# Kernel optimization log

Hardware: AMD Instinct MI355X
Metric: run time of the kernel (lower is better)

The kernel has to match this reference:

```python
import jax, jax.numpy as jnp
import numpy as np

N, D, H, B = 8192, 1024, 100, 32  # pairs, key dim, MLP hidden, batch_size


def setup_inputs() -> dict:
    key = jax.random.key(0)
    ks = jax.random.split(key, 6)
    q = jax.random.normal(ks[0], (N, D), jnp.float32)
    x = jax.random.normal(ks[1], (N, D), jnp.float32)
    b = jax.random.randint(ks[2], (N,), 0, B, dtype=jnp.int32)
    y = jax.random.randint(ks[3], (N,), 0, 2, dtype=jnp.int32)
    # Encoder params: Linear(2D -> H), ReLU, Linear(H -> 1)
    W1 = jax.random.normal(ks[4], (2 * D, H), jnp.float32) * (1.0 / np.sqrt(2 * D))
    b1 = jnp.zeros((H,), jnp.float32)
    W2 = jax.random.normal(ks[5], (H, 1), jnp.float32) * (1.0 / np.sqrt(H))
    b2 = jnp.zeros((1,), jnp.float32)
    return {"b": b, "q": q, "x": x, "y": y, "W1": W1, "b1": b1, "W2": W2, "b2": b2}


def reference(b, q, x, y, W1, b1, W2, b2):
    # Encoder: score per (query, key) pair
    inp = jnp.concatenate([q, x], axis=1)              # (N, 2D)
    h = jax.nn.relu(inp @ W1 + b1)                     # (N, H)
    s = (h @ W2 + b2)[:, 0]                            # (N,)

    n = s.shape[0]
    r = jnp.arange(n)
    yb = y.astype(bool)
    # pair mask: same batch element, differing labels, upper triangle
    m = (b[:, None] == b[None, :]) \
        & (yb[:, None] ^ yb[None, :]) \
        & (r[:, None] < r[None, :])                    # (N, N) bool

    d = s[:, None] - s[None, :]                        # (N, N) score diffs (logits)
    z = y.astype(jnp.float32)[:, None]                 # row label broadcast as target
    # stable BCE-with-logits, masked mean (== BCEWithLogitsLoss over selected pairs)
    bce = jnp.maximum(d, 0.0) - d * z + jnp.log1p(jnp.exp(-jnp.abs(d)))
    mf = m.astype(jnp.float32)
    loss = jnp.sum(bce * mf) / jnp.sum(mf)
    return loss
```

## Files before the change

kernel.cpp:

```cpp
#include <hip/hip_runtime.h>
#include <math.h>
#include <stdint.h>

#define NN 8192
#define DD 1024
#define KT 2048
#define HH 100
#define HP 128
#define LCAP 512
#define NB 32
#define BKC 64
#define NCH (KT / BKC)

typedef short bf16x8 __attribute__((ext_vector_type(8)));
typedef short bf16x4 __attribute__((ext_vector_type(4)));
typedef float f32x4 __attribute__((ext_vector_type(4)));

__device__ __forceinline__ short f2bf(float f) {
    uint32_t u = __builtin_bit_cast(uint32_t, f);
    u += 0x7FFF + ((u >> 16) & 1);
    return (short)(u >> 16);
}

__global__ __launch_bounds__(256) void prep_w1p(const float* __restrict__ W1,
                                                short* __restrict__ w1p)
{
    __shared__ float ld[32][104];
    const int t  = threadIdx.x;
    const int k0 = blockIdx.x * 32;
    for (int i = t; i < 32 * HH; i += 256) {
        const int kk = i / HH, cc = i - kk * HH;
        ld[kk][cc] = W1[(size_t)(k0 + kk) * HH + cc];
    }
    __syncthreads();
    for (int idx = t; idx < 512; idx += 256) {
        const int tt = idx >> 6, l = idx & 63;
        const int lr = l & 15, lg = l >> 4;
        const int col = tt * 16 + lr;
        bf16x8 r;
#pragma unroll
        for (int j = 0; j < 8; ++j)
            r[j] = (col < HH) ? f2bf(ld[lg * 8 + j][col]) : (short)0;
        *(bf16x8*)(w1p + ((size_t)(blockIdx.x * 8 + tt) * 64 + l) * 8) = r;
    }
}

__global__ __launch_bounds__(256) void encoder_mfma(
    const float* __restrict__ q, const float* __restrict__ x,
    const short* __restrict__ w1p,
    const float* __restrict__ b1, const float* __restrict__ W2,
    const float* __restrict__ b2,
    const int* __restrict__ bidx, const int* __restrict__ y,
    float* __restrict__ sp, float* __restrict__ sn,
    int* __restrict__ cnt1, int* __restrict__ cnt0)
{
    __shared__ short As[3][16][64];
    __shared__ float fold[4][16];
    const int t  = threadIdx.x;
    const int w  = t >> 6;
    const int l  = t & 63;
    const int lr = l & 15;
    const int lg = l >> 4;
    const int r0 = blockIdx.x * 16;

    const int srow  = t >> 4;
    const int sslot = t & 15;
    const int wslot = sslot ^ srow;
    const float* qb = q + (size_t)(r0 + srow) * DD + sslot * 4;
    const float* xb = x + (size_t)(r0 + srow) * DD + sslot * 4;
    auto aptr = [&](int c) -> const float* {
        const int kc = c * BKC;
        return (kc < DD) ? (qb + kc) : (xb + (kc - DD));
    };
    auto stage = [&](int buf, const float4& v) {
        bf16x4 s;
        s[0] = f2bf(v.x); s[1] = f2bf(v.y); s[2] = f2bf(v.z); s[3] = f2bf(v.w);
        *(bf16x4*)&As[buf][srow][wslot * 4] = s;
    };

    const int p0 = ((2 * lg)     ^ lr) * 4;
    const int p1 = ((2 * lg + 1) ^ lr) * 4;
    const int p2 = ((2 * lg + 8) ^ lr) * 4;
    const int p3 = ((2 * lg + 9) ^ lr) * 4;

    const short* pB = w1p + ((size_t)(2 * w) * 64 + l) * 8;
#define LOADB(c, x0, x1, x2, x3)                           \
    { const size_t e_ = (size_t)(c) * 8192;                \
      x0 = *(const bf16x8*)(pB + e_);                      \
      x1 = *(const bf16x8*)(pB + e_ + 4096);               \
      x2 = *(const bf16x8*)(pB + e_ + 512);                \
      x3 = *(const bf16x8*)(pB + e_ + 4096 + 512); }

    f32x4 acc0 = (f32x4)0.f, acc1 = (f32x4)0.f;
    bf16x8 bA0, bA1, bA2, bA3, bB0, bB1, bB2, bB3;

#define FRAGS_MFMA(rb, b0, b1_, b2_, b3_)                                   \
    { const short* ar = &As[rb][lr][0];                                     \
      bf16x4 g0 = *(const bf16x4*)(ar + p0);                                \
      bf16x4 g1 = *(const bf16x4*)(ar + p1);                                \
      bf16x4 g2 = *(const bf16x4*)(ar + p2);                                \
      bf16x4 g3 = *(const bf16x4*)(ar + p3);                                \
      bf16x8 aa0 = __builtin_shufflevector(g0, g1, 0,1,2,3,4,5,6,7);        \
      bf16x8 aa1 = __builtin_shufflevector(g2, g3, 0,1,2,3,4,5,6,7);        \
      acc0 = __builtin_amdgcn_mfma_f32_16x16x32_bf16(aa0, b0,  acc0, 0,0,0);\
      acc0 = __builtin_amdgcn_mfma_f32_16x16x32_bf16(aa1, b1_, acc0, 0,0,0);\
      acc1 = __builtin_amdgcn_mfma_f32_16x16x32_bf16(aa0, b2_, acc1, 0,0,0);\
      acc1 = __builtin_amdgcn_mfma_f32_16x16x32_bf16(aa1, b3_, acc1, 0,0,0); }

    float4 t0 = *(const float4*)aptr(0);
    float4 t1 = *(const float4*)aptr(1);
    float4 rE = *(const float4*)aptr(2);
    float4 rO = *(const float4*)aptr(3);
    LOADB(0, bA0, bA1, bA2, bA3);
    stage(0, t0);
    stage(1, t1);
    __syncthreads();

    int rb = 0;
#pragma unroll 1
    for (int c = 0; c < NCH; c += 2) {
        { const int cn = c + 1 < NCH ? c + 1 : NCH - 1; LOADB(cn, bB0, bB1, bB2, bB3); }
        FRAGS_MFMA(rb, bA0, bA1, bA2, bA3);
        __syncthreads();
        { int wb = rb - 1; if (wb < 0) wb = 2;
          stage(wb, rE);
          rE = *(const float4*)aptr(c + 4 < NCH ? c + 4 : NCH - 1); }
        rb = (rb == 2) ? 0 : rb + 1;
        { const int cn = c + 2 < NCH ? c + 2 : NCH - 1; LOADB(cn, bA0, bA1, bA2, bA3); }
        FRAGS_MFMA(rb, bB0, bB1, bB2, bB3);
        __syncthreads();
        { int wb = rb - 1; if (wb < 0) wb = 2;
          stage(wb, rO);
          rO = *(const float4*)aptr(c + 5 < NCH ? c + 5 : NCH - 1); }
        rb = (rb == 2) ? 0 : rb + 1;
    }

    const int c0 = w * 32 + lr;
    const int c1 = c0 + 16;
    const float bb0 = (c0 < HH) ? b1[c0] : 0.f;
    const float ww0 = (c0 < HH) ? W2[c0] : 0.f;
    const float bb1 = (c1 < HH) ? b1[c1] : 0.f;
    const float ww1 = (c1 < HH) ? W2[c1] : 0.f;
#pragma unroll
    for (int r = 0; r < 4; ++r) {
        float v = fmaf(fmaxf(acc0[r] + bb0, 0.f), ww0,
                       fmaxf(acc1[r] + bb1, 0.f) * ww1);
        v += __shfl_xor(v, 1);
        v += __shfl_xor(v, 2);
        v += __shfl_xor(v, 4);
        v += __shfl_xor(v, 8);
        if (lr == 0) fold[w][lg * 4 + r] = v;
    }
    __syncthreads();
    if (t < 16) {
        const float sv = fold[0][t] + fold[1][t] + fold[2][t] + fold[3][t] + b2[0];
        const int i = r0 + t;
        const int g = bidx[i];
        if (y[i]) {
            int idx = atomicAdd(&cnt1[g], 1);
            if (idx < LCAP) sp[g * LCAP + idx] = sv;
        } else {
            int idx = atomicAdd(&cnt0[g], 1);
            if (idx < LCAP) sn[g * LCAP + idx] = sv;
        }
    }
#undef LOADB
#undef FRAGS_MFMA
}

__global__ __launch_bounds__(256) void pairsum_kernel(
    const float* __restrict__ sp, const float* __restrict__ sn,
    const int* __restrict__ cnt1, const int* __restrict__ cnt0,
    float* __restrict__ partial)
{
    __shared__ float lsn[LCAP];
    __shared__ float lsp[64];
    __shared__ float wsum[4];
    const int g  = blockIdx.x >> 3;
    const int sl = blockIdx.x & 7;
    const int t  = threadIdx.x;
    const int n1 = min(cnt1[g], LCAP);
    const int n0 = min(cnt0[g], LCAP);
    for (int j = t; j < n0; j += 256) lsn[j] = sn[g * LCAP + j];
    const int np = (n1 > sl) ? ((n1 - sl + 7) >> 3) : 0;
    for (int j = t; j < np; j += 256) lsp[j] = sp[g * LCAP + sl + j * 8];
    __syncthreads();
    float acc = 0.f;
    const int total = np * n0;
    for (int u = t; u < total; u += 256) {
        const int ip = u / n0;
        const int j  = u - ip * n0;
        const float d  = lsn[j] - lsp[ip];
        const float ad = fabsf(d);
        const float z  = __builtin_exp2f(-ad * 1.44269504f);
        acc += fmaxf(d, 0.f) + __builtin_log2f(1.f + z) * 0.69314718f;
    }
#pragma unroll
    for (int off = 32; off > 0; off >>= 1) acc += __shfl_xor(acc, off, 64);
    const int wid = t >> 6, lane = t & 63;
    if (lane == 0) wsum[wid] = acc;
    __syncthreads();
    if (t == 0) partial[blockIdx.x] = wsum[0] + wsum[1] + wsum[2] + wsum[3];
}

__global__ __launch_bounds__(256) void finalize_kernel(
    const float* __restrict__ partial,
    const int* __restrict__ cnt1, const int* __restrict__ cnt0,
    float* __restrict__ out)
{
    __shared__ float ws_[4], wc_[4];
    const int t = threadIdx.x;
    float sv = partial[t];
    float cv = 0.f;
    if (t < NB) cv = (float)min(cnt1[t], LCAP) * (float)min(cnt0[t], LCAP);
#pragma unroll
    for (int off = 32; off > 0; off >>= 1) {
        sv += __shfl_xor(sv, off, 64);
        cv += __shfl_xor(cv, off, 64);
    }
    const int wid = t >> 6, lane = t & 63;
    if (lane == 0) { ws_[wid] = sv; wc_[wid] = cv; }
    __syncthreads();
    if (t == 0)
        out[0] = (ws_[0] + ws_[1] + ws_[2] + ws_[3]) /
                 (wc_[0] + wc_[1] + wc_[2] + wc_[3]);
}

extern "C" void kernel_launch(void* const* d_in, const int* in_sizes, int n_in,
                              void* d_out, int out_size, void* d_ws, size_t ws_size,
                              hipStream_t stream)
{
    const int*   b  = (const int*)d_in[0];
    const float* q  = (const float*)d_in[1];
    const float* x  = (const float*)d_in[2];
    const int*   y  = (const int*)d_in[3];
    const float* W1 = (const float*)d_in[4];
    const float* b1 = (const float*)d_in[5];
    const float* W2 = (const float*)d_in[6];
    const float* b2 = (const float*)d_in[7];
    float* out = (float*)d_out;

    char* base = (char*)d_ws;
    short* w1p     = (short*)base;
    float* sp      = (float*)(base + 524288);
    float* sn      = (float*)(base + 524288 + 65536);
    int*   cnt1    = (int*)(base + 524288 + 131072);
    int*   cnt0    = cnt1 + NB;
    float* partial = (float*)(base + 524288 + 131072 + 256);

    (void)hipMemsetAsync(cnt1, 0, 2 * NB * sizeof(int), stream);
    prep_w1p<<<KT / 32, 256, 0, stream>>>(W1, w1p);
    encoder_mfma<<<NN / 16, 256, 0, stream>>>(q, x, w1p, b1, W2, b2,
                                              b, y, sp, sn, cnt1, cnt0);
    pairsum_kernel<<<NB * 8, 256, 0, stream>>>(sp, sn, cnt1, cnt0, partial);
    finalize_kernel<<<1, 256, 0, stream>>>(partial, cnt1, cnt0, out);
}
```

Measured before the change: 58.26 us.

## Split encoder GEMM along K into four slices with separate reduction kernel

The encoder's K=2048 reduction is split into four 512-wide slices, so each 16-row tile becomes four blocks and the launch grows from 512 to 2048 blocks. Each block writes its 16x128 partial accumulators to a workspace buffer. A new reduce_score kernel sums the four slices, applies bias, ReLU and W2, and scatters scores by batch and label. This raises parallelism and shortens each block's serial K loop, at the cost of about 16 MB of extra global traffic, an extra kernel launch, and a shorter prefetch pipeline per block.

```diff
diff --git a/kernel.cpp b/kernel.cpp
--- a/kernel.cpp
+++ b/kernel.cpp
@@ -10,7 +10,9 @@
 #define LCAP 512
 #define NB 32
 #define BKC 64
-#define NCH (KT / BKC)
+#define NSL 4
+#define KSL 512
+#define NCHS (KSL / BKC)
 
 typedef short bf16x8 __attribute__((ext_vector_type(8)));
 typedef short bf16x4 __attribute__((ext_vector_type(4)));
@@ -45,33 +47,26 @@
     }
 }
 
-__global__ __launch_bounds__(256) void encoder_mfma(
+__global__ __launch_bounds__(256) void encoder_partial(
     const float* __restrict__ q, const float* __restrict__ x,
-    const short* __restrict__ w1p,
-    const float* __restrict__ b1, const float* __restrict__ W2,
-    const float* __restrict__ b2,
-    const int* __restrict__ bidx, const int* __restrict__ y,
-    float* __restrict__ sp, float* __restrict__ sn,
-    int* __restrict__ cnt1, int* __restrict__ cnt0)
+    const short* __restrict__ w1p, float* __restrict__ part)
 {
     __shared__ short As[3][16][64];
-    __shared__ float fold[4][16];
     const int t  = threadIdx.x;
     const int w  = t >> 6;
     const int l  = t & 63;
     const int lr = l & 15;
     const int lg = l >> 4;
-    const int r0 = blockIdx.x * 16;
+    const int bid   = blockIdx.x;
+    const int slice = bid & 3;
+    const int r0    = (bid >> 2) * 16;
 
     const int srow  = t >> 4;
     const int sslot = t & 15;
     const int wslot = sslot ^ srow;
-    const float* qb = q + (size_t)(r0 + srow) * DD + sslot * 4;
-    const float* xb = x + (size_t)(r0 + srow) * DD + sslot * 4;
-    auto aptr = [&](int c) -> const float* {
-        const int kc = c * BKC;
-        return (kc < DD) ? (qb + kc) : (xb + (kc - DD));
-    };
+    const float* base = ((slice < 2) ? q : x)
+        + (size_t)(r0 + srow) * DD + (slice & 1) * KSL + sslot * 4;
+    auto aptr = [&](int c) -> const float* { return base + c * BKC; };
     auto stage = [&](int buf, const float4& v) {
         bf16x4 s;
         s[0] = f2bf(v.x); s[1] = f2bf(v.y); s[2] = f2bf(v.z); s[3] = f2bf(v.w);
@@ -83,7 +78,8 @@
     const int p2 = ((2 * lg + 8) ^ lr) * 4;
     const int p3 = ((2 * lg + 9) ^ lr) * 4;
 
-    const short* pB = w1p + ((size_t)(2 * w) * 64 + l) * 8;
+    const short* pB = w1p + (size_t)slice * NCHS * 8192
+                    + ((size_t)(2 * w) * 64 + l) * 8;
 #define LOADB(c, x0, x1, x2, x3)                           \
     { const size_t e_ = (size_t)(c) * 8192;                \
       x0 = *(const bf16x8*)(pB + e_);                      \
@@ -118,43 +114,73 @@
 
     int rb = 0;
 #pragma unroll 1
-    for (int c = 0; c < NCH; c += 2) {
-        { const int cn = c + 1 < NCH ? c + 1 : NCH - 1; LOADB(cn, bB0, bB1, bB2, bB3); }
+    for (int c = 0; c < NCHS; c += 2) {
+        { const int cn = c + 1 < NCHS ? c + 1 : NCHS - 1; LOADB(cn, bB0, bB1, bB2, bB3); }
         FRAGS_MFMA(rb, bA0, bA1, bA2, bA3);
         __syncthreads();
         { int wb = rb - 1; if (wb < 0) wb = 2;
           stage(wb, rE);
-          rE = *(const float4*)aptr(c + 4 < NCH ? c + 4 : NCH - 1); }
+          rE = *(const float4*)aptr(c + 4 < NCHS ? c + 4 : NCHS - 1); }
         rb = (rb == 2) ? 0 : rb + 1;
-        { const int cn = c + 2 < NCH ? c + 2 : NCH - 1; LOADB(cn, bA0, bA1, bA2, bA3); }
+        { const int cn = c + 2 < NCHS ? c + 2 : NCHS - 1; LOADB(cn, bA0, bA1, bA2, bA3); }
         FRAGS_MFMA(rb, bB0, bB1, bB2, bB3);
         __syncthreads();
         { int wb = rb - 1; if (wb < 0) wb = 2;
           stage(wb, rO);
-          rO = *(const float4*)aptr(c + 5 < NCH ? c + 5 : NCH - 1); }
+          rO = *(const float4*)aptr(c + 5 < NCHS ? c + 5 : NCHS - 1); }
         rb = (rb == 2) ? 0 : rb + 1;
     }
 
-    const int c0 = w * 32 + lr;
-    const int c1 = c0 + 16;
-    const float bb0 = (c0 < HH) ? b1[c0] : 0.f;
-    const float ww0 = (c0 < HH) ? W2[c0] : 0.f;
-    const float bb1 = (c1 < HH) ? b1[c1] : 0.f;
-    const float ww1 = (c1 < HH) ? W2[c1] : 0.f;
+    float* pp = part + ((size_t)slice * NN + r0) * HP;
 #pragma unroll
     for (int r = 0; r < 4; ++r) {
-        float v = fmaf(fmaxf(acc0[r] + bb0, 0.f), ww0,
-                       fmaxf(acc1[r] + bb1, 0.f) * ww1);
-        v += __shfl_xor(v, 1);
-        v += __shfl_xor(v, 2);
-        v += __shfl_xor(v, 4);
-        v += __shfl_xor(v, 8);
-        if (lr == 0) fold[w][lg * 4 + r] = v;
-    }
-    __syncthreads();
-    if (t < 16) {
-        const float sv = fold[0][t] + fold[1][t] + fold[2][t] + fold[3][t] + b2[0];
-        const int i = r0 + t;
+        const int row = lg * 4 + r;
+        pp[row * HP + w * 32 + lr]      = acc0[r];
+        pp[row * HP + w * 32 + lr + 16] = acc1[r];
+    }
+#undef LOADB
+#undef FRAGS_MFMA
+}
+
+__global__ __launch_bounds__(256) void reduce_score(
+    const float* __restrict__ part,
+    const float* __restrict__ b1, const float* __restrict__ W2,
+    const float* __restrict__ b2,
+    const int* __restrict__ bidx, const int* __restrict__ y,
+    float* __restrict__ sp, float* __restrict__ sn,
+    int* __restrict__ cnt1, int* __restrict__ cnt0)
+{
+    const int t   = threadIdx.x;
+    const int row = t >> 4;
+    const int cg  = t & 15;
+    const int c0  = cg * 8;
+    const int r0  = blockIdx.x * 16;
+    const float* pr = part + ((size_t)(r0 + row)) * HP + c0;
+    f32x4 s0 = (f32x4)0.f, s1 = (f32x4)0.f;
+#pragma unroll
+    for (int sl = 0; sl < NSL; ++sl) {
+        const float* p = pr + (size_t)sl * NN * HP;
+        s0 += *(const f32x4*)p;
+        s1 += *(const f32x4*)(p + 4);
+    }
+    float acc = 0.f;
+#pragma unroll
+    for (int j = 0; j < 4; ++j) {
+        const int ca = c0 + j, cb = c0 + 4 + j;
+        const float ba = (ca < HH) ? b1[ca] : 0.f;
+        const float wa = (ca < HH) ? W2[ca] : 0.f;
+        const float bb = (cb < HH) ? b1[cb] : 0.f;
+        const float wb = (cb < HH) ? W2[cb] : 0.f;
+        acc = fmaf(fmaxf(s0[j] + ba, 0.f), wa, acc);
+        acc = fmaf(fmaxf(s1[j] + bb, 0.f), wb, acc);
+    }
+    acc += __shfl_xor(acc, 1);
+    acc += __shfl_xor(acc, 2);
+    acc += __shfl_xor(acc, 4);
+    acc += __shfl_xor(acc, 8);
+    if (cg == 0) {
+        const float sv = acc + b2[0];
+        const int i = r0 + row;
         const int g = bidx[i];
         if (y[i]) {
             int idx = atomicAdd(&cnt1[g], 1);
@@ -164,8 +190,6 @@
             if (idx < LCAP) sn[g * LCAP + idx] = sv;
         }
     }
-#undef LOADB
-#undef FRAGS_MFMA
 }
 
 __global__ __launch_bounds__(256) void pairsum_kernel(
@@ -247,10 +271,12 @@
     int*   cnt1    = (int*)(base + 524288 + 131072);
     int*   cnt0    = cnt1 + NB;
     float* partial = (float*)(base + 524288 + 131072 + 256);
+    float* part    = (float*)(base + 1048576);
 
     (void)hipMemsetAsync(cnt1, 0, 2 * NB * sizeof(int), stream);
     prep_w1p<<<KT / 32, 256, 0, stream>>>(W1, w1p);
-    encoder_mfma<<<NN / 16, 256, 0, stream>>>(q, x, w1p, b1, W2, b2,
+    encoder_partial<<<(NN / 16) * NSL, 256, 0, stream>>>(q, x, w1p, part);
+    reduce_score<<<NN / 16, 256, 0, stream>>>(part, b1, W2, b2,
                                               b, y, sp, sn, cnt1, cnt0);
     pairsum_kernel<<<NB * 8, 256, 0, stream>>>(sp, sn, cnt1, cnt0, partial);
     finalize_kernel<<<1, 256, 0, stream>>>(partial, cnt1, cnt0, out);
```

Result: slower. 74.23 us (+27.4%).

## Split encoder K-reduction across two wave groups and fold memset into prep kernel

Applied to the files above, without the earlier changes.

The encoder block grows to 512 threads: one group of four waves reduces over the q half of the concatenated input and the other over the x half, each with its own LDS ring buffer and W1 slice. The two partial hidden accumulators are combined in shared memory before the bias, ReLU and W2 dot. This halves the serial K-loop per block and doubles the waves available to hide latency, at the cost of extra LDS, two more barriers and lower block occupancy. The counter memset is also moved into prep_w1p to save one queued operation.

```diff
diff --git a/kernel.cpp b/kernel.cpp
--- a/kernel.cpp
+++ b/kernel.cpp
@@ -10,7 +10,7 @@
 #define LCAP 512
 #define NB 32
 #define BKC 64
-#define NCH (KT / BKC)
+#define NBH 16
 
 typedef short bf16x8 __attribute__((ext_vector_type(8)));
 typedef short bf16x4 __attribute__((ext_vector_type(4)));
@@ -23,10 +23,15 @@
 }
 
 __global__ __launch_bounds__(256) void prep_w1p(const float* __restrict__ W1,
-                                                short* __restrict__ w1p)
+                                                short* __restrict__ w1p,
+                                                int* __restrict__ cnt1,
+                                                int* __restrict__ cnt0)
 {
     __shared__ float ld[32][104];
     const int t  = threadIdx.x;
+    if (blockIdx.x == 0 && t < 64) {
+        if (t < 32) cnt1[t] = 0; else cnt0[t - 32] = 0;
+    }
     const int k0 = blockIdx.x * 32;
     for (int i = t; i < 32 * HH; i += 256) {
         const int kk = i / HH, cc = i - kk * HH;
@@ -45,7 +50,7 @@
     }
 }
 
-__global__ __launch_bounds__(256) void encoder_mfma(
+__global__ __launch_bounds__(512) void encoder_mfma(
     const float* __restrict__ q, const float* __restrict__ x,
     const short* __restrict__ w1p,
     const float* __restrict__ b1, const float* __restrict__ W2,
@@ -54,28 +59,27 @@
     float* __restrict__ sp, float* __restrict__ sn,
     int* __restrict__ cnt1, int* __restrict__ cnt0)
 {
-    __shared__ short As[3][16][64];
-    __shared__ float fold[4][16];
-    const int t  = threadIdx.x;
-    const int w  = t >> 6;
-    const int l  = t & 63;
-    const int lr = l & 15;
-    const int lg = l >> 4;
-    const int r0 = blockIdx.x * 16;
-
-    const int srow  = t >> 4;
-    const int sslot = t & 15;
+    __shared__ short As[2][3][16][64];
+    __shared__ float fold[8][16];
+    const int t    = threadIdx.x;
+    const int w    = t >> 6;
+    const int half = w >> 2;
+    const int wc   = w & 3;
+    const int l    = t & 63;
+    const int lr   = l & 15;
+    const int lg   = l >> 4;
+    const int r0   = blockIdx.x * 16;
+
+    const int ts    = t & 255;
+    const int srow  = ts >> 4;
+    const int sslot = ts & 15;
     const int wslot = sslot ^ srow;
-    const float* qb = q + (size_t)(r0 + srow) * DD + sslot * 4;
-    const float* xb = x + (size_t)(r0 + srow) * DD + sslot * 4;
-    auto aptr = [&](int c) -> const float* {
-        const int kc = c * BKC;
-        return (kc < DD) ? (qb + kc) : (xb + (kc - DD));
-    };
+    const float* abase = (half ? x : q) + (size_t)(r0 + srow) * DD + sslot * 4;
+    auto aptr  = [&](int c) -> const float* { return abase + c * BKC; };
     auto stage = [&](int buf, const float4& v) {
         bf16x4 s;
         s[0] = f2bf(v.x); s[1] = f2bf(v.y); s[2] = f2bf(v.z); s[3] = f2bf(v.w);
-        *(bf16x4*)&As[buf][srow][wslot * 4] = s;
+        *(bf16x4*)&As[half][buf][srow][wslot * 4] = s;
     };
 
     const int p0 = ((2 * lg)     ^ lr) * 4;
@@ -83,7 +87,8 @@
     const int p2 = ((2 * lg + 8) ^ lr) * 4;
     const int p3 = ((2 * lg + 9) ^ lr) * 4;
 
-    const short* pB = w1p + ((size_t)(2 * w) * 64 + l) * 8;
+    const short* pB = w1p + (size_t)half * NBH * 8192
+                    + ((size_t)(2 * wc) * 64 + l) * 8;
 #define LOADB(c, x0, x1, x2, x3)                           \
     { const size_t e_ = (size_t)(c) * 8192;                \
       x0 = *(const bf16x8*)(pB + e_);                      \
@@ -95,7 +100,7 @@
     bf16x8 bA0, bA1, bA2, bA3, bB0, bB1, bB2, bB3;
 
 #define FRAGS_MFMA(rb, b0, b1_, b2_, b3_)                                   \
-    { const short* ar = &As[rb][lr][0];                                     \
+    { const short* ar = &As[half][rb][lr][0];                               \
       bf16x4 g0 = *(const bf16x4*)(ar + p0);                                \
       bf16x4 g1 = *(const bf16x4*)(ar + p1);                                \
       bf16x4 g2 = *(const bf16x4*)(ar + p2);                                \
@@ -118,38 +123,58 @@
 
     int rb = 0;
 #pragma unroll 1
-    for (int c = 0; c < NCH; c += 2) {
-        { const int cn = c + 1 < NCH ? c + 1 : NCH - 1; LOADB(cn, bB0, bB1, bB2, bB3); }
+    for (int c = 0; c < NBH; c += 2) {
+        { const int cn = c + 1 < NBH ? c + 1 : NBH - 1; LOADB(cn, bB0, bB1, bB2, bB3); }
         FRAGS_MFMA(rb, bA0, bA1, bA2, bA3);
         __syncthreads();
         { int wb = rb - 1; if (wb < 0) wb = 2;
           stage(wb, rE);
-          rE = *(const float4*)aptr(c + 4 < NCH ? c + 4 : NCH - 1); }
+          rE = *(const float4*)aptr(c + 4 < NBH ? c + 4 : NBH - 1); }
         rb = (rb == 2) ? 0 : rb + 1;
-        { const int cn = c + 2 < NCH ? c + 2 : NCH - 1; LOADB(cn, bA0, bA1, bA2, bA3); }
+        { const int cn = c + 2 < NBH ? c + 2 : NBH - 1; LOADB(cn, bA0, bA1, bA2, bA3); }
         FRAGS_MFMA(rb, bB0, bB1, bB2, bB3);
         __syncthreads();
         { int wb = rb - 1; if (wb < 0) wb = 2;
           stage(wb, rO);
-          rO = *(const float4*)aptr(c + 5 < NCH ? c + 5 : NCH - 1); }
+          rO = *(const float4*)aptr(c + 5 < NBH ? c + 5 : NBH - 1); }
         rb = (rb == 2) ? 0 : rb + 1;
     }
 
-    const int c0 = w * 32 + lr;
-    const int c1 = c0 + 16;
-    const float bb0 = (c0 < HH) ? b1[c0] : 0.f;
-    const float ww0 = (c0 < HH) ? W2[c0] : 0.f;
-    const float bb1 = (c1 < HH) ? b1[c1] : 0.f;
-    const float ww1 = (c1 < HH) ? W2[c1] : 0.f;
-#pragma unroll
-    for (int r = 0; r < 4; ++r) {
-        float v = fmaf(fmaxf(acc0[r] + bb0, 0.f), ww0,
-                       fmaxf(acc1[r] + bb1, 0.f) * ww1);
-        v += __shfl_xor(v, 1);
-        v += __shfl_xor(v, 2);
-        v += __shfl_xor(v, 4);
-        v += __shfl_xor(v, 8);
-        if (lr == 0) fold[w][lg * 4 + r] = v;
+    __shared__ float hsum[16][HP + 4];
+    if (half == 0) {
+#pragma unroll
+        for (int r = 0; r < 4; ++r) {
+            hsum[lg * 4 + r][wc * 32 + lr]      = acc0[r];
+            hsum[lg * 4 + r][wc * 32 + lr + 16] = acc1[r];
+        }
+    }
+    __syncthreads();
+    if (half == 1) {
+#pragma unroll
+        for (int r = 0; r < 4; ++r) {
+            hsum[lg * 4 + r][wc * 32 + lr]      += acc0[r];
+            hsum[lg * 4 + r][wc * 32 + lr + 16] += acc1[r];
+        }
+    }
+    __syncthreads();
+    if (half == 0) {
+        const int c0 = wc * 32 + lr;
+        const int c1 = c0 + 16;
+        const float bb0 = (c0 < HH) ? b1[c0] : 0.f;
+        const float ww0 = (c0 < HH) ? W2[c0] : 0.f;
+        const float bb1 = (c1 < HH) ? b1[c1] : 0.f;
+        const float ww1 = (c1 < HH) ? W2[c1] : 0.f;
+#pragma unroll
+        for (int r = 0; r < 4; ++r) {
+            const int row = lg * 4 + r;
+            float v = fmaf(fmaxf(hsum[row][c0] + bb0, 0.f), ww0,
+                           fmaxf(hsum[row][c1] + bb1, 0.f) * ww1);
+            v += __shfl_xor(v, 1);
+            v += __shfl_xor(v, 2);
+            v += __shfl_xor(v, 4);
+            v += __shfl_xor(v, 8);
+            if (lr == 0) fold[wc][row] = v;
+        }
     }
     __syncthreads();
     if (t < 16) {
@@ -248,9 +273,8 @@
     int*   cnt0    = cnt1 + NB;
     float* partial = (float*)(base + 524288 + 131072 + 256);
 
-    (void)hipMemsetAsync(cnt1, 0, 2 * NB * sizeof(int), stream);
-    prep_w1p<<<KT / 32, 256, 0, stream>>>(W1, w1p);
-    encoder_mfma<<<NN / 16, 256, 0, stream>>>(q, x, w1p, b1, W2, b2,
+    prep_w1p<<<KT / 32, 256, 0, stream>>>(W1, w1p, cnt1, cnt0);
+    encoder_mfma<<<NN / 16, 512, 0, stream>>>(q, x, w1p, b1, W2, b2,
                                               b, y, sp, sn, cnt1, cnt0);
     pairsum_kernel<<<NB * 8, 256, 0, stream>>>(sp, sn, cnt1, cnt0, partial);
     finalize_kernel<<<1, 256, 0, stream>>>(partial, cnt1, cnt0, out);
```

Result: faster. 49.70 us (-14.7%).
